# Performance work log

Measured on AMD Instinct MI355X. Metric: run time of the kernel, lower is better.

Reference implementation:

```python
import jax, jax.numpy as jnp
import numpy as np

NUM_HEADS = 8


def _rel_to_abs(x):
    # x: [b, h, l, 2l-1] relative logits -> [b, h, l, l] absolute logits
    b, h, l, _ = x.shape
    x = jnp.pad(x, ((0, 0), (0, 0), (0, 0), (0, 1)))          # [b,h,l,2l]
    x = x.reshape(b, h, l * 2 * l)
    x = jnp.pad(x, ((0, 0), (0, 0), (0, l - 1)))               # [b,h,2l^2+l-1]
    x = x.reshape(b, h, l + 1, 2 * l - 1)
    return x[:, :, :l, l - 1:]                                 # [b,h,l,l]


def setup_inputs() -> dict:
    key = jax.random.key(0)
    k1, k2, k3 = jax.random.split(key, 3)
    B, H, D, L = 8, NUM_HEADS, 64, 512
    std = D ** (-0.5)
    qkv = jax.random.normal(k1, (B, 3 * H * D, L), dtype=jnp.float32)
    k_emb = jax.random.normal(k2, (H, 2 * L - 1, D), dtype=jnp.float32) * std
    v_emb = jax.random.normal(k3, (H, 2 * L - 1, D), dtype=jnp.float32) * std
    return {"qkv": qkv, "k_emb": k_emb, "v_emb": v_emb}


def reference(qkv, k_emb, v_emb):
    # qkv: [B, 3*H*D, L]; k_emb/v_emb: [H, 2L-1, D]
    B, C3, L = qkv.shape
    H = NUM_HEADS
    D = C3 // (3 * H)
    x = qkv.reshape(B, H, 3 * D, L)
    q = jnp.transpose(x[:, :, :D, :], (0, 1, 3, 2))          # [B,H,L,D]
    k = jnp.transpose(x[:, :, D:2 * D, :], (0, 1, 3, 2))
    v = jnpp = jnp.transpose(x[:, :, 2 * D:, :], (0, 1, 3, 2))
    logits = jnp.einsum('bhld,bhmd->bhlm', q, k)             # [B,H,L,L] (no 1/sqrt(d) scale in original)
    rel_logits = jnp.einsum('bhld,hmd->bhlm', q, k_emb)      # [B,H,L,2L-1]
    logits = logits + _rel_to_abs(rel_logits)
    weights = jax.nn.softmax(logits, axis=-1)
    out = jnp.einsum('bhlm,bhmd->bhld', weights, v)          # [B,H,L,D]
    # add_relative_to_values=False in module, so v_emb is unused (parameter only)
    return out.reshape(B, -1, L)                              # [B, H*D, L] via raw reshape, as in torch
```

## Files before the change

kernel.cpp:

```cpp
#include <hip/hip_runtime.h>
#include <hip/hip_bf16.h>

#define NH 8
#define DH 64
#define SL 512

typedef __bf16 bf16x8 __attribute__((ext_vector_type(8)));
typedef float f32x16 __attribute__((ext_vector_type(16)));
typedef float f32x4 __attribute__((ext_vector_type(4)));
typedef unsigned int u32;

#define MFMA(a, b, c) __builtin_amdgcn_mfma_f32_32x32x16_bf16(a, b, c, 0, 0, 0)
#define ZERO16 {0.f,0.f,0.f,0.f,0.f,0.f,0.f,0.f,0.f,0.f,0.f,0.f,0.f,0.f,0.f,0.f}

__device__ __forceinline__ void split8(const f32x4 a, const f32x4 b, bf16x8& h8, bf16x8& l8) {
    union { __hip_bfloat16 s[8]; bf16x8 v; } uh, ul;
#pragma unroll
    for (int i = 0; i < 4; ++i) {
        __hip_bfloat16 h0 = __float2bfloat16(a[i]);
        __hip_bfloat16 h1 = __float2bfloat16(b[i]);
        uh.s[i] = h0; uh.s[4 + i] = h1;
        ul.s[i]     = __float2bfloat16(a[i] - __bfloat162float(h0));
        ul.s[4 + i] = __float2bfloat16(b[i] - __bfloat162float(h1));
    }
    h8 = uh.v; l8 = ul.v;
}
__device__ __forceinline__ void cvt8(const f32x4 a, const f32x4 b, bf16x8& h8) {
    union { __hip_bfloat16 s[8]; bf16x8 v; } uh;
#pragma unroll
    for (int i = 0; i < 4; ++i) {
        uh.s[i]     = __float2bfloat16(a[i]);
        uh.s[4 + i] = __float2bfloat16(b[i]);
    }
    h8 = uh.v;
}

__device__ __forceinline__ float ldv(const __hip_bfloat16* p) { return __bfloat162float(*p); }
__device__ __forceinline__ void stv(__hip_bfloat16* p, float v) { *p = __float2bfloat16(v); }

__global__ __launch_bounds__(256, 2) void attn_fused(
    const void* __restrict__ qkv_v,
    const void* __restrict__ k_emb_v,
    void* __restrict__ out_v)
{
    const int t = threadIdx.x;
    const int bid = blockIdx.x;

    __shared__ int s_flag;
    {
        unsigned int u = (unsigned int)((const unsigned short*)qkv_v)[t];
        float f = __uint_as_float(u << 16);
        bool big = !(fabsf(f) <= 1e4f);
        unsigned long long vote = __ballot(big);
        if (t == 0) s_flag = 0;
        __syncthreads();
        if (vote != 0ull && (t & 63) == 0) atomicOr(&s_flag, 1);
        __syncthreads();
    }
    const bool is_f32 = (s_flag != 0);

    __shared__ float srect[4][2048];
    __shared__ float sstat[4][2][32];
    __shared__ float s_w[SL];
    __shared__ float s_red[24];
    __shared__ float s_part[256];
    __shared__ float s_q[DH];

    if (is_f32) {
        const float* qkv   = (const float*)qkv_v;
        const float* k_emb = (const float*)k_emb_v;
        float* out         = (float*)out_v;

        const int h    = bid & 7;
        const int rest = bid >> 3;
        const int b    = rest & 7;
        const int lt   = rest >> 3;
        const int bh   = b * NH + h;
        const int wid = t >> 6, lane = t & 63;
        const int lo = lane & 31, hi = lane >> 5;
        const int mq = wid;
        const int l0 = lt * 32;

        const float* qbase = qkv + (size_t)bh * (3 * DH * SL);
        const float* kglob = qbase + DH * SL;
        const float* vflat = qbase + (size_t)2 * DH * SL;
        const float* ebase = k_emb + (size_t)h * (2 * SL - 1) * DH;

        bf16x8 qfh[4], qfl[4];
#pragma unroll
        for (int ds = 0; ds < 4; ++ds) {
            const float* qp = qbase + (size_t)(16 * ds + 8 * hi) * SL + (l0 + lo);
            f32x4 xa, xb;
#pragma unroll
            for (int i = 0; i < 4; ++i) { xa[i] = qp[(size_t)i * SL]; xb[i] = qp[(size_t)(4 + i) * SL]; }
            split8(xa, xb, qfh[ds], qfl[ds]);
        }

        const int rb0 = mq * 128 - l0 + 480;
        bf16x8 eah[4];
        {
            const float* e0p = ebase + (size_t)(rb0 + lo) * DH;
#pragma unroll
            for (int ds = 0; ds < 4; ++ds) {
                const int off = 16 * ds + 8 * hi;
                cvt8(*(const f32x4*)(e0p + off), *(const f32x4*)(e0p + off + 4), eah[ds]);
            }
        }

        float* rect = srect[wid];
        float* rrow = rect + lo * 64;
        const int sw = (lo & 7) << 2;

        f32x16 o0 = ZERO16, o1 = ZERO16;
        float mx = -1e30f, sum = 0.f;

        for (int step = 0; step < 4; ++step) {
            const int m0 = mq * 128 + step * 32;
            const int rb = rb0 + step * 32;

            bf16x8 kh[4], kl[4];
#pragma unroll
            for (int ds = 0; ds < 4; ++ds) {
                const float* kp = kglob + (size_t)(16 * ds + 8 * hi) * SL + (m0 + lo);
                f32x4 xa, xb;
#pragma unroll
                for (int i = 0; i < 4; ++i) { xa[i] = kp[(size_t)i * SL]; xb[i] = kp[(size_t)(4 + i) * SL]; }
                split8(xa, xb, kh[ds], kl[ds]);
            }
            bf16x8 ech[4];
            {
                int r1 = rb + 32 + lo; if (r1 > 1022) r1 = 1022;
                const float* e1p = ebase + (size_t)r1 * DH;
#pragma unroll
                for (int ds = 0; ds < 4; ++ds) {
                    const int off = 16 * ds + 8 * hi;
                    cvt8(*(const f32x4*)(e1p + off), *(const f32x4*)(e1p + off + 4), ech[ds]);
                }
            }
            const float* v0p = vflat + (size_t)lo * SL + m0 + 8 * hi;
            const float* v1p = vflat + (size_t)(32 + lo) * SL + m0 + 8 * hi;
            bf16x8 v00h, v00l, v01h, v01l, v10h, v10l, v11h, v11l;
            split8(*(const f32x4*)v0p,        *(const f32x4*)(v0p + 4),  v00h, v00l);
            split8(*(const f32x4*)(v0p + 16), *(const f32x4*)(v0p + 20), v01h, v01l);
            split8(*(const f32x4*)v1p,        *(const f32x4*)(v1p + 4),  v10h, v10l);
            split8(*(const f32x4*)(v1p + 16), *(const f32x4*)(v1p + 20), v11h, v11l);

            f32x16 ra = ZERO16, rc = ZERO16, sacc = ZERO16;
            __builtin_amdgcn_s_setprio(1);
#pragma unroll
            for (int ds = 0; ds < 4; ++ds) {
                sacc = MFMA(kh[ds], qfh[ds], sacc);
                sacc = MFMA(kh[ds], qfl[ds], sacc);
                sacc = MFMA(kl[ds], qfh[ds], sacc);
                ra   = MFMA(eah[ds], qfh[ds], ra);
                rc   = MFMA(ech[ds], qfh[ds], rc);
            }
            __builtin_amdgcn_s_setprio(0);

#pragma unroll
            for (int g = 0; g < 4; ++g) {
                const int j0 = 8 * g + 4 * hi;
                f32x4 w0 = { ra[4 * g], ra[4 * g + 1], ra[4 * g + 2], ra[4 * g + 3] };
                f32x4 w1 = { rc[4 * g], rc[4 * g + 1], rc[4 * g + 2], rc[4 * g + 3] };
                *(f32x4*)(rrow + (j0 ^ sw))        = w0;
                *(f32x4*)(rrow + ((j0 + 32) ^ sw)) = w1;
            }
            float s[16];
#pragma unroll
            for (int r = 0; r < 16; ++r) {
                const int mp = (r & 3) + 8 * (r >> 2) + 4 * hi;
                s[r] = sacc[r] + rrow[(mp + 31 - lo) ^ sw];
            }

            float tmx = s[0];
#pragma unroll
            for (int r = 1; r < 16; ++r) tmx = fmaxf(tmx, s[r]);
            tmx = fmaxf(tmx, __shfl_xor(tmx, 32, 64));
            if (!__all(tmx <= mx + 8.f)) {
                const float nmx = fmaxf(mx, tmx);
                const float sc = __expf(mx - nmx);
#pragma unroll
                for (int r = 0; r < 16; ++r) { o0[r] *= sc; o1[r] *= sc; }
                sum *= sc;
                mx = nmx;
            }
            u32 pk[8], xk[8];
            float ps = 0.f;
#pragma unroll
            for (int q2 = 0; q2 < 8; ++q2) {
                union { __hip_bfloat162 b2; u32 u; } cv;
                cv.b2 = __float22bfloat162_rn(make_float2(__expf(s[2 * q2] - mx),
                                                          __expf(s[2 * q2 + 1] - mx)));
                pk[q2] = cv.u;
                float2 g2 = __bfloat1622float2(cv.b2);
                ps += g2.x + g2.y;
            }
            sum += ps;
#pragma unroll
            for (int q2 = 0; q2 < 8; ++q2) xk[q2] = (u32)__shfl_xor((int)pk[q2], 32, 64);

            union { u32 u[4]; bf16x8 v; } pf0, pf1;
            if (hi == 0) {
                pf0.u[0] = pk[0]; pf0.u[1] = pk[1]; pf0.u[2] = xk[0]; pf0.u[3] = xk[1];
                pf1.u[0] = pk[4]; pf1.u[1] = pk[5]; pf1.u[2] = xk[4]; pf1.u[3] = xk[5];
            } else {
                pf0.u[0] = xk[2]; pf0.u[1] = xk[3]; pf0.u[2] = pk[2]; pf0.u[3] = pk[3];
                pf1.u[0] = xk[6]; pf1.u[1] = xk[7]; pf1.u[2] = pk[6]; pf1.u[3] = pk[7];
            }
            __builtin_amdgcn_s_setprio(1);
            o0 = MFMA(v00h, pf0.v, o0);
            o0 = MFMA(v00l, pf0.v, o0);
            o0 = MFMA(v01h, pf1.v, o0);
            o0 = MFMA(v01l, pf1.v, o0);
            o1 = MFMA(v10h, pf0.v, o1);
            o1 = MFMA(v10l, pf0.v, o1);
            o1 = MFMA(v11h, pf1.v, o1);
            o1 = MFMA(v11l, pf1.v, o1);
            __builtin_amdgcn_s_setprio(0);

#pragma unroll
            for (int ds = 0; ds < 4; ++ds) eah[ds] = ech[ds];
        }

        sum += __shfl_xor(sum, 32, 64);

        if (wid > 0) {
            if (hi == 0) { sstat[wid][0][lo] = mx; sstat[wid][1][lo] = sum; }
            float* ob = rect;
#pragma unroll
            for (int r = 0; r < 16; ++r) {
                const int d0 = (r & 3) + 8 * (r >> 2) + 4 * hi;
                ob[d0 * 32 + lo]        = o0[r];
                ob[(32 + d0) * 32 + lo] = o1[r];
            }
        }
        __syncthreads();
        if (wid == 0) {
            const float m1 = sstat[1][0][lo], s1 = sstat[1][1][lo];
            const float m2 = sstat[2][0][lo], s2 = sstat[2][1][lo];
            const float m3 = sstat[3][0][lo], s3 = sstat[3][1][lo];
            const float nm = fmaxf(fmaxf(mx, m1), fmaxf(m2, m3));
            const float a0 = __expf(mx - nm);
            const float a1 = __expf(m1 - nm);
            const float a2 = __expf(m2 - nm);
            const float a3 = __expf(m3 - nm);
            const float inv = 1.f / (a0 * sum + a1 * s1 + a2 * s2 + a3 * s3);
            const float* ob1 = srect[1];
            const float* ob2 = srect[2];
            const float* ob3 = srect[3];
            float* orow = out + ((size_t)bh * SL + l0 + lo) * DH;
#pragma unroll
            for (int r = 0; r < 16; r += 2) {
                const int d0 = (r & 3) + 8 * (r >> 2) + 4 * hi;
                float2 w0 = make_float2(
                    (a0 * o0[r]     + a1 * ob1[d0 * 32 + lo] + a2 * ob2[d0 * 32 + lo] + a3 * ob3[d0 * 32 + lo]) * inv,
                    (a0 * o0[r + 1] + a1 * ob1[(d0 + 1) * 32 + lo] + a2 * ob2[(d0 + 1) * 32 + lo] + a3 * ob3[(d0 + 1) * 32 + lo]) * inv);
                *(float2*)(orow + d0) = w0;
                float2 w1 = make_float2(
                    (a0 * o1[r]     + a1 * ob1[(32 + d0) * 32 + lo] + a2 * ob2[(32 + d0) * 32 + lo] + a3 * ob3[(32 + d0) * 32 + lo]) * inv,
                    (a0 * o1[r + 1] + a1 * ob1[(32 + d0 + 1) * 32 + lo] + a2 * ob2[(32 + d0 + 1) * 32 + lo] + a3 * ob3[(32 + d0 + 1) * 32 + lo]) * inv);
                *(float2*)(orow + 32 + d0) = w1;
            }
        }
    } else {
        const __hip_bfloat16* qkv   = (const __hip_bfloat16*)qkv_v;
        const __hip_bfloat16* k_emb = (const __hip_bfloat16*)k_emb_v;
        __hip_bfloat16* out         = (__hip_bfloat16*)out_v;

        for (int it = 0; it < 32; ++it) {
            const int row = bid * 32 + it;
            const int l   = row & (SL - 1);
            const int bh  = row >> 9;
            const int h   = bh & (NH - 1);
            const long base = (long)bh * (3 * DH) * SL;

            __syncthreads();
            if (t < DH) s_q[t] = ldv(&qkv[base + (long)t * SL + l]);
            __syncthreads();

            const __hip_bfloat16* kp = qkv + base + (long)DH * SL;
            const __hip_bfloat16* ke = k_emb + (long)h * (2 * SL - 1) * DH;
            float lg[2];
#pragma unroll
            for (int i = 0; i < 2; ++i) {
                const int m = t + i * 256;
                float acc = 0.f;
#pragma unroll 8
                for (int d = 0; d < DH; ++d)
                    acc += s_q[d] * ldv(&kp[(long)d * SL + m]);
                const int r = m - l + (SL - 1);
                const __hip_bfloat16* kr = ke + (long)r * DH;
                float acc2 = 0.f;
#pragma unroll 8
                for (int d = 0; d < DH; ++d)
                    acc2 += s_q[d] * ldv(&kr[d]);
                lg[i] = acc + acc2;
            }

            float mxv = fmaxf(lg[0], lg[1]);
            for (int off = 32; off > 0; off >>= 1)
                mxv = fmaxf(mxv, __shfl_down(mxv, off, 64));
            if ((t & 63) == 0) s_red[t >> 6] = mxv;
            __syncthreads();
            if (t == 0)
                s_red[8] = fmaxf(fmaxf(s_red[0], s_red[1]), fmaxf(s_red[2], s_red[3]));
            __syncthreads();
            mxv = s_red[8];

            const float e0 = expf(lg[0] - mxv);
            const float e1 = expf(lg[1] - mxv);
            s_w[t] = e0;
            s_w[t + 256] = e1;
            float sm = e0 + e1;
            for (int off = 32; off > 0; off >>= 1)
                sm += __shfl_down(sm, off, 64);
            if ((t & 63) == 0) s_red[16 + (t >> 6)] = sm;
            __syncthreads();
            const float inv = 1.0f / (s_red[16] + s_red[17] + s_red[18] + s_red[19]);

            const __hip_bfloat16* vp = qkv + base + (long)(2 * DH) * SL;
            const int g  = t >> 6;
            const int dd = t & 63;
            const __hip_bfloat16* vrow = vp + (long)dd * SL + g * 128;
            const float* wrow = s_w + g * 128;
            float acc = 0.f;
#pragma unroll 8
            for (int m = 0; m < 128; ++m)
                acc += wrow[m] * ldv(&vrow[m]);
            s_part[t] = acc;
            __syncthreads();
            if (t < 64) {
                float o = (s_part[t] + s_part[t + 64] + s_part[t + 128] + s_part[t + 192]) * inv;
                stv(&out[((long)bh * SL + l) * DH + t], o);
            }
        }
    }
}

extern "C" void kernel_launch(void* const* d_in, const int* in_sizes, int n_in,
                              void* d_out, int out_size, void* d_ws, size_t ws_size,
                              hipStream_t stream) {
    (void)in_sizes; (void)n_in; (void)out_size; (void)d_ws; (void)ws_size;
    attn_fused<<<1024, 256, 0, stream>>>(d_in[0], d_in[1], d_out);
}
```

Before: 116.1 us.

## Split key range across eight waves per block instead of four

```diff
diff --git a/kernel.cpp b/kernel.cpp
--- a/kernel.cpp
+++ b/kernel.cpp
@@ -38,7 +38,7 @@
 __device__ __forceinline__ float ldv(const __hip_bfloat16* p) { return __bfloat162float(*p); }
 __device__ __forceinline__ void stv(__hip_bfloat16* p, float v) { *p = __float2bfloat16(v); }
 
-__global__ __launch_bounds__(256, 2) void attn_fused(
+__global__ __launch_bounds__(512, 4) void attn_fused(
     const void* __restrict__ qkv_v,
     const void* __restrict__ k_emb_v,
     void* __restrict__ out_v)
@@ -59,11 +59,11 @@
     }
     const bool is_f32 = (s_flag != 0);
 
-    __shared__ float srect[4][2048];
-    __shared__ float sstat[4][2][32];
+    __shared__ float srect[8][2048];
+    __shared__ float sstat[8][2][32];
     __shared__ float s_w[SL];
     __shared__ float s_red[24];
-    __shared__ float s_part[256];
+    __shared__ float s_part[512];
     __shared__ float s_q[DH];
 
     if (is_f32) {
@@ -78,8 +78,8 @@
         const int bh   = b * NH + h;
         const int wid = t >> 6, lane = t & 63;
         const int lo = lane & 31, hi = lane >> 5;
-        const int mq = wid;
         const int l0 = lt * 32;
+        const int mbase = wid * 64;
 
         const float* qbase = qkv + (size_t)bh * (3 * DH * SL);
         const float* kglob = qbase + DH * SL;
@@ -96,7 +96,7 @@
             split8(xa, xb, qfh[ds], qfl[ds]);
         }
 
-        const int rb0 = mq * 128 - l0 + 480;
+        const int rb0 = mbase - l0 + 480;
         bf16x8 eah[4];
         {
             const float* e0p = ebase + (size_t)(rb0 + lo) * DH;
@@ -114,8 +114,8 @@
         f32x16 o0 = ZERO16, o1 = ZERO16;
         float mx = -1e30f, sum = 0.f;
 
-        for (int step = 0; step < 4; ++step) {
-            const int m0 = mq * 128 + step * 32;
+        for (int step = 0; step < 2; ++step) {
+            const int m0 = mbase + step * 32;
             const int rb = rb0 + step * 32;
 
             bf16x8 kh[4], kl[4];
@@ -176,8 +176,8 @@
 #pragma unroll
             for (int r = 1; r < 16; ++r) tmx = fmaxf(tmx, s[r]);
             tmx = fmaxf(tmx, __shfl_xor(tmx, 32, 64));
-            if (!__all(tmx <= mx + 8.f)) {
-                const float nmx = fmaxf(mx, tmx);
+            const float nmx = fmaxf(mx, tmx);
+            if (__any(nmx > mx)) {
                 const float sc = __expf(mx - nmx);
 #pragma unroll
                 for (int r = 0; r < 16; ++r) { o0[r] *= sc; o1[r] *= sc; }
@@ -236,30 +236,34 @@
         }
         __syncthreads();
         if (wid == 0) {
-            const float m1 = sstat[1][0][lo], s1 = sstat[1][1][lo];
-            const float m2 = sstat[2][0][lo], s2 = sstat[2][1][lo];
-            const float m3 = sstat[3][0][lo], s3 = sstat[3][1][lo];
-            const float nm = fmaxf(fmaxf(mx, m1), fmaxf(m2, m3));
-            const float a0 = __expf(mx - nm);
-            const float a1 = __expf(m1 - nm);
-            const float a2 = __expf(m2 - nm);
-            const float a3 = __expf(m3 - nm);
-            const float inv = 1.f / (a0 * sum + a1 * s1 + a2 * s2 + a3 * s3);
-            const float* ob1 = srect[1];
-            const float* ob2 = srect[2];
-            const float* ob3 = srect[3];
+            float pm[8], psum[8];
+            pm[0] = mx; psum[0] = sum;
+            float nm = mx;
+#pragma unroll
+            for (int w = 1; w < 8; ++w) {
+                pm[w] = sstat[w][0][lo]; psum[w] = sstat[w][1][lo];
+                nm = fmaxf(nm, pm[w]);
+            }
+            float aw[8], tot = 0.f;
+#pragma unroll
+            for (int w = 0; w < 8; ++w) { aw[w] = __expf(pm[w] - nm); tot += aw[w] * psum[w]; }
+            const float inv = 1.f / tot;
             float* orow = out + ((size_t)bh * SL + l0 + lo) * DH;
 #pragma unroll
             for (int r = 0; r < 16; r += 2) {
                 const int d0 = (r & 3) + 8 * (r >> 2) + 4 * hi;
-                float2 w0 = make_float2(
-                    (a0 * o0[r]     + a1 * ob1[d0 * 32 + lo] + a2 * ob2[d0 * 32 + lo] + a3 * ob3[d0 * 32 + lo]) * inv,
-                    (a0 * o0[r + 1] + a1 * ob1[(d0 + 1) * 32 + lo] + a2 * ob2[(d0 + 1) * 32 + lo] + a3 * ob3[(d0 + 1) * 32 + lo]) * inv);
-                *(float2*)(orow + d0) = w0;
-                float2 w1 = make_float2(
-                    (a0 * o1[r]     + a1 * ob1[(32 + d0) * 32 + lo] + a2 * ob2[(32 + d0) * 32 + lo] + a3 * ob3[(32 + d0) * 32 + lo]) * inv,
-                    (a0 * o1[r + 1] + a1 * ob1[(32 + d0 + 1) * 32 + lo] + a2 * ob2[(32 + d0 + 1) * 32 + lo] + a3 * ob3[(32 + d0 + 1) * 32 + lo]) * inv);
-                *(float2*)(orow + 32 + d0) = w1;
+                float acc00 = aw[0] * o0[r],     acc01 = aw[0] * o0[r + 1];
+                float acc10 = aw[0] * o1[r],     acc11 = aw[0] * o1[r + 1];
+#pragma unroll
+                for (int w = 1; w < 8; ++w) {
+                    const float* ob = srect[w];
+                    acc00 += aw[w] * ob[d0 * 32 + lo];
+                    acc01 += aw[w] * ob[(d0 + 1) * 32 + lo];
+                    acc10 += aw[w] * ob[(32 + d0) * 32 + lo];
+                    acc11 += aw[w] * ob[(32 + d0 + 1) * 32 + lo];
+                }
+                *(float2*)(orow + d0)      = make_float2(acc00 * inv, acc01 * inv);
+                *(float2*)(orow + 32 + d0) = make_float2(acc10 * inv, acc11 * inv);
             }
         }
     } else {
@@ -280,58 +284,58 @@
 
             const __hip_bfloat16* kp = qkv + base + (long)DH * SL;
             const __hip_bfloat16* ke = k_emb + (long)h * (2 * SL - 1) * DH;
-            float lg[2];
-#pragma unroll
-            for (int i = 0; i < 2; ++i) {
-                const int m = t + i * 256;
-                float acc = 0.f;
+            const int m = t;
+            float acc = 0.f;
 #pragma unroll 8
-                for (int d = 0; d < DH; ++d)
-                    acc += s_q[d] * ldv(&kp[(long)d * SL + m]);
-                const int r = m - l + (SL - 1);
-                const __hip_bfloat16* kr = ke + (long)r * DH;
-                float acc2 = 0.f;
+            for (int d = 0; d < DH; ++d)
+                acc += s_q[d] * ldv(&kp[(long)d * SL + m]);
+            const int r = m - l + (SL - 1);
+            const __hip_bfloat16* kr = ke + (long)r * DH;
+            float acc2 = 0.f;
 #pragma unroll 8
-                for (int d = 0; d < DH; ++d)
-                    acc2 += s_q[d] * ldv(&kr[d]);
-                lg[i] = acc + acc2;
-            }
-
-            float mxv = fmaxf(lg[0], lg[1]);
+            for (int d = 0; d < DH; ++d)
+                acc2 += s_q[d] * ldv(&kr[d]);
+            const float lg = acc + acc2;
+
+            float mxv = lg;
             for (int off = 32; off > 0; off >>= 1)
                 mxv = fmaxf(mxv, __shfl_down(mxv, off, 64));
             if ((t & 63) == 0) s_red[t >> 6] = mxv;
             __syncthreads();
-            if (t == 0)
-                s_red[8] = fmaxf(fmaxf(s_red[0], s_red[1]), fmaxf(s_red[2], s_red[3]));
+            if (t == 0) {
+                float m8 = s_red[0];
+                for (int w = 1; w < 8; ++w) m8 = fmaxf(m8, s_red[w]);
+                s_red[8] = m8;
+            }
             __syncthreads();
             mxv = s_red[8];
 
-            const float e0 = expf(lg[0] - mxv);
-            const float e1 = expf(lg[1] - mxv);
+            const float e0 = expf(lg - mxv);
             s_w[t] = e0;
-            s_w[t + 256] = e1;
-            float sm = e0 + e1;
+            float sm = e0;
             for (int off = 32; off > 0; off >>= 1)
                 sm += __shfl_down(sm, off, 64);
             if ((t & 63) == 0) s_red[16 + (t >> 6)] = sm;
             __syncthreads();
-            const float inv = 1.0f / (s_red[16] + s_red[17] + s_red[18] + s_red[19]);
+            float tot = 0.f;
+            for (int w = 0; w < 8; ++w) tot += s_red[16 + w];
+            const float inv = 1.0f / tot;
 
             const __hip_bfloat16* vp = qkv + base + (long)(2 * DH) * SL;
             const int g  = t >> 6;
             const int dd = t & 63;
-            const __hip_bfloat16* vrow = vp + (long)dd * SL + g * 128;
-            const float* wrow = s_w + g * 128;
-            float acc = 0.f;
+            const __hip_bfloat16* vrow = vp + (long)dd * SL + g * 64;
+            const float* wrow = s_w + g * 64;
+            float pacc = 0.f;
 #pragma unroll 8
-            for (int m = 0; m < 128; ++m)
-                acc += wrow[m] * ldv(&vrow[m]);
-            s_part[t] = acc;
+            for (int mm = 0; mm < 64; ++mm)
+                pacc += wrow[mm] * ldv(&vrow[mm]);
+            s_part[t] = pacc;
             __syncthreads();
             if (t < 64) {
-                float o = (s_part[t] + s_part[t + 64] + s_part[t + 128] + s_part[t + 192]) * inv;
-                stv(&out[((long)bh * SL + l) * DH + t], o);
+                float o = 0.f;
+                for (int w = 0; w < 8; ++w) o += s_part[t + 64 * w];
+                stv(&out[((long)bh * SL + l) * DH + t], o * inv);
             }
         }
     }
@@ -341,5 +345,5 @@
                               void* d_out, int out_size, void* d_ws, size_t ws_size,
                               hipStream_t stream) {
     (void)in_sizes; (void)n_in; (void)out_size; (void)d_ws; (void)ws_size;
-    attn_fused<<<1024, 256, 0, stream>>>(d_in[0], d_in[1], d_out);
+    attn_fused<<<1024, 512, 0, stream>>>(d_in[0], d_in[1], d_out);
 }
```

New measurement: 297.6 us. +156.4%, slower.
